# Optimization experiments

Hardware: AMD Instinct MI355X
Metric: run time of the kernel (lower is better)

Reference implementation:

```python
import jax, jax.numpy as jnp
import numpy as np


def gcn_conv(x, src, dst, W, b, N):
    """PyG GCNConv: add self-loops, symmetric D^-1/2 (A+I) D^-1/2 normalization."""
    loop = jnp.arange(N, dtype=src.dtype)
    s = jnp.concatenate([src, loop])
    d = jnp.concatenate([dst, loop])
    deg = jnp.zeros((N,), dtype=x.dtype).at[d].add(1.0)  # in-degree incl. self-loop
    dinv = jax.lax.rsqrt(deg)  # deg >= 1 because of self-loops
    norm = dinv[s] * dinv[d]  # [E+N]
    h = x @ W  # [N, out] linear transform first (as in PyG)
    msg = h[s] * norm[:, None]  # gather + scale
    out = jax.ops.segment_sum(msg, d, num_segments=N)  # scatter-add
    return out + b


def setup_inputs() -> dict:
    key = jax.random.key(0)
    ks = jax.random.split(key, 10)
    N, E, in_dim, h1, h2, A = 100000, 3200000, 256, 32, 64, 64
    x = jax.random.normal(ks[0], (N, in_dim), dtype=jnp.float32)
    ei = jax.random.randint(ks[1], (2, E), 0, N, dtype=jnp.int64)
    def glorot(k, shape):
        lim = float(np.sqrt(6.0 / (shape[0] + shape[1])))
        return jax.random.uniform(k, shape, jnp.float32, -lim, lim)
    return {
        "x": x,
        "ei": ei,
        "num_nodes": N,
        "W1": glorot(ks[2], (in_dim, h1)), "b1": jnp.zeros((h1,), jnp.float32),
        "W2": glorot(ks[3], (h1, h2)),     "b2": jnp.zeros((h2,), jnp.float32),
        "Wo1": glorot(ks[4], (h2, h2)),    "bo1": jnp.zeros((h2,), jnp.float32),
        "Wo2": glorot(ks[5], (h2, A)),     "bo2": jnp.zeros((A,), jnp.float32),
    }


def reference(x, ei, num_nodes, W1, b1, W2, b2, Wo1, bo1, Wo2, bo2):
    src, dst = ei[0], ei[1]
    z = jax.nn.relu(gcn_conv(x, src, dst, W1, b1, num_nodes))
    z = jax.nn.relu(gcn_conv(z, src, dst, W2, b2, num_nodes))
    logits = jax.nn.relu(z @ Wo1 + bo1) @ Wo2 + bo2  # [N, action_space]
    nbatches = z.shape[0] // num_nodes
    # original reshapes with z.size(1)=hidden2 (== action_space here)
    dist = logits.reshape(nbatches, num_nodes * z.shape[1])
    return jax.nn.softmax(dist, axis=-1)  # Categorical probs
```

## Files before the change

### kernel.cpp

```cpp
#include <hip/hip_runtime.h>

#define DEVI __device__ __forceinline__

DEVI unsigned fkey(float f) {
  unsigned u = __float_as_uint(f);
  return u ^ ((u >> 31) ? 0xFFFFFFFFu : 0x80000000u);
}
DEVI float funkey(unsigned k) {
  unsigned b = (k & 0x80000000u) ? (k ^ 0x80000000u) : ~k;
  return __uint_as_float(b);
}
DEVI float f4get(const float4& v, int j) {
  return j == 0 ? v.x : j == 1 ? v.y : j == 2 ? v.z : v.w;
}

constexpr int BSH = 9;
constexpr int BNODES = 1 << BSH;
constexpr int PEPT = 16;
constexpr int PCHUNK = 256 * PEPT;

__global__ void k_binit(int* __restrict__ bcnt) {
  bcnt[threadIdx.x] = 0;
}

__global__ void k_bcount(const int* __restrict__ dst, int* __restrict__ bcnt,
                         int E, int NB) {
  __shared__ int lh[256];
  lh[threadIdx.x] = 0;
  __syncthreads();
  int stride = gridDim.x * 256;
  for (long i = (long)blockIdx.x * 256 + threadIdx.x; i < E; i += stride)
    atomicAdd(&lh[dst[i] >> BSH], 1);
  __syncthreads();
  if (threadIdx.x < NB && lh[threadIdx.x]) atomicAdd(&bcnt[threadIdx.x], lh[threadIdx.x]);
}

__global__ void k_bscan(const int* __restrict__ bcnt, int* __restrict__ bbase,
                        int* __restrict__ bcur, unsigned* __restrict__ scal, int NB) {
  __shared__ int s[256];
  int t = threadIdx.x;
  int v = (t < NB) ? bcnt[t] : 0;
  s[t] = v;
  __syncthreads();
  for (int o = 1; o < 256; o <<= 1) {
    int add = (t >= o) ? s[t - o] : 0;
    __syncthreads();
    s[t] += add;
    __syncthreads();
  }
  int excl = s[t] - v;
  if (t < NB) { bbase[t] = excl; bcur[t] = excl; }
  if (t == 0) { scal[0] = 0u; scal[1] = 0u; }
}

__global__ __launch_bounds__(256)
void k_bpart(const int* __restrict__ src, const int* __restrict__ dst,
             int* __restrict__ bcur, unsigned* __restrict__ epart, int E, int NB) {
  __shared__ int lh[256];
  __shared__ int gbase[256];
  long base = (long)blockIdx.x * PCHUNK;
  lh[threadIdx.x] = 0;
  __syncthreads();
  int ed[PEPT]; int es[PEPT]; unsigned short lpos[PEPT];
#pragma unroll
  for (int j = 0; j < PEPT; j++) {
    long i = base + threadIdx.x + (long)j * 256;
    if (i < E) {
      int d = dst[i];
      es[j] = src[i];
      ed[j] = d;
      lpos[j] = (unsigned short)atomicAdd(&lh[d >> BSH], 1);
    } else {
      ed[j] = -1;
    }
  }
  __syncthreads();
  if (threadIdx.x < NB) {
    int c = lh[threadIdx.x];
    gbase[threadIdx.x] = c ? atomicAdd(&bcur[threadIdx.x], c) : 0;
  }
  __syncthreads();
#pragma unroll
  for (int j = 0; j < PEPT; j++) {
    int d = ed[j];
    if (d >= 0) {
      unsigned p = (unsigned)(gbase[d >> BSH] + (int)lpos[j]);
      epart[p] = ((unsigned)(d & (BNODES - 1)) << 17) | (unsigned)es[j];
    }
  }
}

__global__ __launch_bounds__(256)
void k_fine(const unsigned* __restrict__ epart, const int* __restrict__ bbase,
            const int* __restrict__ bcnt, int* __restrict__ rowptr,
            int* __restrict__ deg, float* __restrict__ dinv,
            int* __restrict__ col, int N) {
  __shared__ int lh[BNODES];
  __shared__ int lexcl[BNODES];
  __shared__ int ssc[256];
  int b = blockIdx.x;
  int base = bbase[b], cnt = bcnt[b];
  int nlo = b << BSH;
  int t = threadIdx.x;
  lh[t] = 0; lh[t + 256] = 0;
  __syncthreads();
  for (int i = t; i < cnt; i += 256) {
    unsigned e = epart[base + i];
    atomicAdd(&lh[e >> 17], 1);
  }
  __syncthreads();
  int a0 = lh[2 * t], a1 = lh[2 * t + 1];
  ssc[t] = a0 + a1;
  __syncthreads();
  for (int o = 1; o < 256; o <<= 1) {
    int add = (t >= o) ? ssc[t - o] : 0;
    __syncthreads();
    ssc[t] += add;
    __syncthreads();
  }
  int excl = ssc[t] - (a0 + a1);
  lexcl[2 * t] = excl;
  lexcl[2 * t + 1] = excl + a0;
  __syncthreads();
#pragma unroll
  for (int k = 0; k < 2; k++) {
    int i = t + k * 256;
    int v = nlo + i;
    if (v < N) {
      int dgv = lh[i];
      deg[v] = dgv;
      rowptr[v] = base + lexcl[i];
      dinv[v] = rsqrtf((float)(dgv + 1));
    }
  }
  __syncthreads();
  lh[2 * t] = lexcl[2 * t];
  lh[2 * t + 1] = lexcl[2 * t + 1];
  __syncthreads();
  for (int i = t; i < cnt; i += 256) {
    unsigned e = epart[base + i];
    int p = atomicAdd(&lh[e >> 17], 1);
    col[base + p] = (int)(e & 0x1FFFFu);
  }
}

__global__ __launch_bounds__(256)
void k_gemm1(const float* __restrict__ in, const float* __restrict__ W,
             const float* __restrict__ dinv, float* __restrict__ out, int N) {
  __shared__ float Wl[256 * 32];
  __shared__ float xb[2][128 * 16];
  const int t = threadIdx.x;

  {
    const float4* W4 = (const float4*)W;
    float4* Wl4 = (float4*)Wl;
#pragma unroll
    for (int i = 0; i < 8; i++) Wl4[t + i * 256] = W4[t + i * 256];
  }

  const int srow = t >> 1;
  const int part = t & 1;
  const int sk = (srow >> 1) & 3;
  long grow = (long)blockIdx.x * 128 + srow;
  const float* gsrc = in + (grow < (long)N ? grow : (long)(N - 1)) * 256 + part * 8;
  const int q0 = part * 2, q1 = part * 2 + 1;
  const int ws0 = srow * 16 + ((q0 ^ sk) << 2);
  const int ws1 = srow * 16 + ((q1 ^ sk) << 2);

  const int cg = t & 3;
  const int rg = t >> 2;
  const int c0 = cg * 8;
  const int rk = (rg >> 1) & 3;

  {
    float4 a = *(const float4*)(gsrc + 0);
    float4 b = *(const float4*)(gsrc + 4);
    *(float4*)&xb[0][ws0] = a;
    *(float4*)&xb[0][ws1] = b;
  }
  __syncthreads();

  float acc[2][8];
#pragma unroll
  for (int i = 0; i < 2; i++)
#pragma unroll
    for (int c = 0; c < 8; c++) acc[i][c] = 0.f;

  for (int ch = 0; ch < 16; ch++) {
    float4 na, nb;
    if (ch < 15) {
      na = *(const float4*)(gsrc + (ch + 1) * 16 + 0);
      nb = *(const float4*)(gsrc + (ch + 1) * 16 + 4);
    }
    const float* xc = xb[ch & 1];
#pragma unroll
    for (int q = 0; q < 4; q++) {
      float4 xv0 = *(const float4*)&xc[rg * 16 + ((q ^ rk) << 2)];
      float4 xv1 = *(const float4*)&xc[(rg + 64) * 16 + ((q ^ rk) << 2)];
#pragma unroll
      for (int jj = 0; jj < 4; jj++) {
        const float* wr = &Wl[(ch * 16 + q * 4 + jj) * 32 + c0];
        float4 wa = *(const float4*)(wr);
        float4 wb = *(const float4*)(wr + 4);
        float x0 = f4get(xv0, jj);
        float x1 = f4get(xv1, jj);
        acc[0][0] = fmaf(x0, wa.x, acc[0][0]);
        acc[0][1] = fmaf(x0, wa.y, acc[0][1]);
        acc[0][2] = fmaf(x0, wa.z, acc[0][2]);
        acc[0][3] = fmaf(x0, wa.w, acc[0][3]);
        acc[0][4] = fmaf(x0, wb.x, acc[0][4]);
        acc[0][5] = fmaf(x0, wb.y, acc[0][5]);
        acc[0][6] = fmaf(x0, wb.z, acc[0][6]);
        acc[0][7] = fmaf(x0, wb.w, acc[0][7]);
        acc[1][0] = fmaf(x1, wa.x, acc[1][0]);
        acc[1][1] = fmaf(x1, wa.y, acc[1][1]);
        acc[1][2] = fmaf(x1, wa.z, acc[1][2]);
        acc[1][3] = fmaf(x1, wa.w, acc[1][3]);
        acc[1][4] = fmaf(x1, wb.x, acc[1][4]);
        acc[1][5] = fmaf(x1, wb.y, acc[1][5]);
        acc[1][6] = fmaf(x1, wb.z, acc[1][6]);
        acc[1][7] = fmaf(x1, wb.w, acc[1][7]);
      }
    }
    if (ch < 15) {
      __syncthreads();
      float* xn = xb[(ch + 1) & 1];
      *(float4*)&xn[ws0] = na;
      *(float4*)&xn[ws1] = nb;
      __syncthreads();
    }
  }

#pragma unroll
  for (int i = 0; i < 2; i++) {
    long r = (long)blockIdx.x * 128 + rg + i * 64;
    if (r < (long)N) {
      float dv = dinv[r];
      float* op = &out[r * 32 + c0];
      *(float4*)(op) = make_float4(acc[i][0] * dv, acc[i][1] * dv,
                                   acc[i][2] * dv, acc[i][3] * dv);
      *(float4*)(op + 4) = make_float4(acc[i][4] * dv, acc[i][5] * dv,
                                       acc[i][6] * dv, acc[i][7] * dv);
    }
  }
}

__global__ __launch_bounds__(256)
void k_head(const float* __restrict__ s2,
            const float* __restrict__ W2, const float* __restrict__ b2,
            const float* __restrict__ Wo1, const float* __restrict__ bo1,
            const float* __restrict__ Wo2, const float* __restrict__ bo2,
            float* __restrict__ out, int N, unsigned* __restrict__ gmax) {
  __shared__ float A[64 * 64];
  __shared__ float B[64 * 64];
  __shared__ float xr[128 * 64];
  const int t = threadIdx.x;
  const int cg = t & 7, rg = t >> 3;
  const int c0 = cg * 8;
  const int key = rg & 7;
  const long r0 = (long)blockIdx.x * 128 + rg * 4;

  {
    const float4* w2 = (const float4*)W2;
    const float4* w1 = (const float4*)Wo1;
    float4* Af = (float4*)A;
    float4* Bf = (float4*)B;
    Af[t] = w2[t];
    Af[t + 256] = w2[t + 256];
#pragma unroll
    for (int i = 0; i < 4; i++) Bf[t + i * 256] = w1[t + i * 256];
  }
  __syncthreads();

  bool rv[4];
  int xrow[4];
#pragma unroll
  for (int i = 0; i < 4; i++) {
    rv[i] = (r0 + i) < (long)N;
    xrow[i] = (rg + 32 * i) * 64;
  }
  const int q0 = (2 * cg) ^ key, q1 = (2 * cg + 1) ^ key;

  float a1[4][8], a2[4][8];

#pragma unroll
  for (int i = 0; i < 4; i++)
#pragma unroll
    for (int c = 0; c < 8; c++) a1[i][c] = 0.f;
  {
    const float* ip = s2 + r0 * 32;
#pragma unroll 2
    for (int k = 0; k < 32; k += 4) {
      float4 xv[4];
#pragma unroll
      for (int i = 0; i < 4; i++)
        xv[i] = rv[i] ? *(const float4*)(ip + i * 32 + k)
                      : make_float4(0.f, 0.f, 0.f, 0.f);
#pragma unroll
      for (int jj = 0; jj < 4; jj++) {
        float4 wa = *(const float4*)&A[(k + jj) * 64 + c0];
        float4 wb = *(const float4*)&A[(k + jj) * 64 + c0 + 4];
#pragma unroll
        for (int i = 0; i < 4; i++) {
          float xs = f4get(xv[i], jj);
          a1[i][0] = fmaf(xs, wa.x, a1[i][0]);
          a1[i][1] = fmaf(xs, wa.y, a1[i][1]);
          a1[i][2] = fmaf(xs, wa.z, a1[i][2]);
          a1[i][3] = fmaf(xs, wa.w, a1[i][3]);
          a1[i][4] = fmaf(xs, wb.x, a1[i][4]);
          a1[i][5] = fmaf(xs, wb.y, a1[i][5]);
          a1[i][6] = fmaf(xs, wb.z, a1[i][6]);
          a1[i][7] = fmaf(xs, wb.w, a1[i][7]);
        }
      }
    }
    float bo[8];
#pragma unroll
    for (int c = 0; c < 8; c++) bo[c] = b2[c0 + c];
#pragma unroll
    for (int i = 0; i < 4; i++) {
      float v0 = fmaxf(a1[i][0] + bo[0], 0.f);
      float v1 = fmaxf(a1[i][1] + bo[1], 0.f);
      float v2 = fmaxf(a1[i][2] + bo[2], 0.f);
      float v3 = fmaxf(a1[i][3] + bo[3], 0.f);
      float v4 = fmaxf(a1[i][4] + bo[4], 0.f);
      float v5 = fmaxf(a1[i][5] + bo[5], 0.f);
      float v6 = fmaxf(a1[i][6] + bo[6], 0.f);
      float v7 = fmaxf(a1[i][7] + bo[7], 0.f);
      *(float4*)&xr[xrow[i] + 4 * q0] = make_float4(v0, v1, v2, v3);
      *(float4*)&xr[xrow[i] + 4 * q1] = make_float4(v4, v5, v6, v7);
    }
  }
  __syncthreads();

  float4 wn[4];
  {
    const float4* w = (const float4*)Wo2;
#pragma unroll
    for (int i = 0; i < 4; i++) wn[i] = w[t + i * 256];
  }

#pragma unroll
  for (int i = 0; i < 4; i++)
#pragma unroll
    for (int c = 0; c < 8; c++) a2[i][c] = 0.f;
#pragma unroll 2
  for (int k = 0; k < 64; k += 4) {
    const int q = k >> 2;
    float4 xv[4];
#pragma unroll
    for (int i = 0; i < 4; i++)
      xv[i] = *(const float4*)&xr[xrow[i] + 4 * (q ^ key)];
#pragma unroll
    for (int jj = 0; jj < 4; jj++) {
      float4 wa = *(const float4*)&B[(k + jj) * 64 + c0];
      float4 wb = *(const float4*)&B[(k + jj) * 64 + c0 + 4];
#pragma unroll
      for (int i = 0; i < 4; i++) {
        float xs = f4get(xv[i], jj);
        a2[i][0] = fmaf(xs, wa.x, a2[i][0]);
        a2[i][1] = fmaf(xs, wa.y, a2[i][1]);
        a2[i][2] = fmaf(xs, wa.z, a2[i][2]);
        a2[i][3] = fmaf(xs, wa.w, a2[i][3]);
        a2[i][4] = fmaf(xs, wb.x, a2[i][4]);
        a2[i][5] = fmaf(xs, wb.y, a2[i][5]);
        a2[i][6] = fmaf(xs, wb.z, a2[i][6]);
        a2[i][7] = fmaf(xs, wb.w, a2[i][7]);
      }
    }
  }
  __syncthreads();

  {
    float4* Af = (float4*)A;
#pragma unroll
    for (int i = 0; i < 4; i++) Af[t + i * 256] = wn[i];
    float bo[8];
#pragma unroll
    for (int c = 0; c < 8; c++) bo[c] = bo1[c0 + c];
#pragma unroll
    for (int i = 0; i < 4; i++) {
      float v0 = fmaxf(a2[i][0] + bo[0], 0.f);
      float v1 = fmaxf(a2[i][1] + bo[1], 0.f);
      float v2 = fmaxf(a2[i][2] + bo[2], 0.f);
      float v3 = fmaxf(a2[i][3] + bo[3], 0.f);
      float v4 = fmaxf(a2[i][4] + bo[4], 0.f);
      float v5 = fmaxf(a2[i][5] + bo[5], 0.f);
      float v6 = fmaxf(a2[i][6] + bo[6], 0.f);
      float v7 = fmaxf(a2[i][7] + bo[7], 0.f);
      *(float4*)&xr[xrow[i] + 4 * q0] = make_float4(v0, v1, v2, v3);
      *(float4*)&xr[xrow[i] + 4 * q1] = make_float4(v4, v5, v6, v7);
    }
  }
  __syncthreads();

#pragma unroll
  for (int i = 0; i < 4; i++)
#pragma unroll
    for (int c = 0; c < 8; c++) a1[i][c] = 0.f;
#pragma unroll 2
  for (int k = 0; k < 64; k += 4) {
    const int q = k >> 2;
    float4 xv[4];
#pragma unroll
    for (int i = 0; i < 4; i++)
      xv[i] = *(const float4*)&xr[xrow[i] + 4 * (q ^ key)];
#pragma unroll
    for (int jj = 0; jj < 4; jj++) {
      float4 wa = *(const float4*)&A[(k + jj) * 64 + c0];
      float4 wb = *(const float4*)&A[(k + jj) * 64 + c0 + 4];
#pragma unroll
      for (int i = 0; i < 4; i++) {
        float xs = f4get(xv[i], jj);
        a1[i][0] = fmaf(xs, wa.x, a1[i][0]);
        a1[i][1] = fmaf(xs, wa.y, a1[i][1]);
        a1[i][2] = fmaf(xs, wa.z, a1[i][2]);
        a1[i][3] = fmaf(xs, wa.w, a1[i][3]);
        a1[i][4] = fmaf(xs, wb.x, a1[i][4]);
        a1[i][5] = fmaf(xs, wb.y, a1[i][5]);
        a1[i][6] = fmaf(xs, wb.z, a1[i][6]);
        a1[i][7] = fmaf(xs, wb.w, a1[i][7]);
      }
    }
  }

  float m = -3.4e38f;
  {
    float bo[8];
#pragma unroll
    for (int c = 0; c < 8; c++) bo[c] = bo2[c0 + c];
#pragma unroll
    for (int i = 0; i < 4; i++) {
      if (!rv[i]) continue;
      float o[8];
#pragma unroll
      for (int c = 0; c < 8; c++) {
        float v = a1[i][c] + bo[c];
        m = fmaxf(m, v);
        o[c] = v;
      }
      float* op = &out[(r0 + i) * 64 + c0];
      *(float4*)(op) = make_float4(o[0], o[1], o[2], o[3]);
      *(float4*)(op + 4) = make_float4(o[4], o[5], o[6], o[7]);
    }
  }
#pragma unroll
  for (int o2 = 1; o2 < 64; o2 <<= 1) m = fmaxf(m, __shfl_xor(m, o2, 64));
  if ((t & 63) == 0) atomicMax(gmax, fkey(m));
}

template <int FEAT, bool BIAS, bool RELU, bool PSCALE>
__launch_bounds__(256)
__global__ void k_aggv(const float* __restrict__ g, const int* __restrict__ col,
                       const int* __restrict__ rowptr, const int* __restrict__ deg,
                       const float* __restrict__ dinv, const float* __restrict__ bias,
                       float* __restrict__ out, int N) {
  constexpr int LPN = FEAT / 4;
  constexpr int NPB = 256 / LPN;
  int nib = threadIdx.x / LPN;
  int c = threadIdx.x % LPN;
  long v = (long)blockIdx.x * NPB + nib;
  if (v >= N) return;

  const float4* g4 = (const float4*)g;
  float4 acc = g4[v * LPN + c];
  int start = rowptr[v], dg = deg[v];
  int e = 0;
  while (e < dg) {
    int cnt = min(LPN, dg - e);
    int idx = (c < cnt) ? col[start + e + c] : 0;
    int j = 0;
    for (; j + 4 <= cnt; j += 4) {
      int u0 = __shfl(idx, j + 0, LPN);
      int u1 = __shfl(idx, j + 1, LPN);
      int u2 = __shfl(idx, j + 2, LPN);
      int u3 = __shfl(idx, j + 3, LPN);
      float4 a0 = g4[(long)u0 * LPN + c];
      float4 a1 = g4[(long)u1 * LPN + c];
      float4 a2 = g4[(long)u2 * LPN + c];
      float4 a3 = g4[(long)u3 * LPN + c];
      acc.x += (a0.x + a1.x) + (a2.x + a3.x);
      acc.y += (a0.y + a1.y) + (a2.y + a3.y);
      acc.z += (a0.z + a1.z) + (a2.z + a3.z);
      acc.w += (a0.w + a1.w) + (a2.w + a3.w);
    }
    for (; j < cnt; j++) {
      int u = __shfl(idx, j, LPN);
      float4 a = g4[(long)u * LPN + c];
      acc.x += a.x; acc.y += a.y; acc.z += a.z; acc.w += a.w;
    }
    e += cnt;
  }
  float dv = dinv[v];
  float4 val;
  val.x = acc.x * dv; val.y = acc.y * dv; val.z = acc.z * dv; val.w = acc.w * dv;
  if (BIAS) {
    float4 b = ((const float4*)bias)[c];
    val.x += b.x; val.y += b.y; val.z += b.z; val.w += b.w;
  }
  if (RELU) {
    val.x = fmaxf(val.x, 0.f); val.y = fmaxf(val.y, 0.f);
    val.z = fmaxf(val.z, 0.f); val.w = fmaxf(val.w, 0.f);
  }
  if (PSCALE) {
    val.x *= dv; val.y *= dv; val.z *= dv; val.w *= dv;
  }
  ((float4*)out)[v * LPN + c] = val;
}

__global__ void k_smsum(const float* __restrict__ logit, unsigned* __restrict__ scal, int total) {
  __shared__ float s[256];
  float gmax = funkey(scal[0]);
  float loc = 0.f;
  for (int i = blockIdx.x * 256 + threadIdx.x; i < total; i += gridDim.x * 256)
    loc += expf(logit[i] - gmax);
  s[threadIdx.x] = loc; __syncthreads();
  for (int o = 128; o > 0; o >>= 1) {
    if (threadIdx.x < o) s[threadIdx.x] += s[threadIdx.x + o];
    __syncthreads();
  }
  if (threadIdx.x == 0) atomicAdd((float*)&scal[1], s[0]);
}

__global__ void k_smnorm(float* __restrict__ logit, const unsigned* __restrict__ scal, int total) {
  float gmax = funkey(scal[0]);
  float inv = 1.0f / __uint_as_float(scal[1]);
  int i = blockIdx.x * 256 + threadIdx.x;
  if (i < total) logit[i] = expf(logit[i] - gmax) * inv;
}

extern "C" void kernel_launch(void* const* d_in, const int* in_sizes, int n_in,
                              void* d_out, int out_size, void* d_ws, size_t ws_size,
                              hipStream_t stream) {
  const float* x   = (const float*)d_in[0];
  const int*   ei  = (const int*)d_in[1];
  const float* W1  = (const float*)d_in[3];
  const float* b1  = (const float*)d_in[4];
  const float* W2  = (const float*)d_in[5];
  const float* b2  = (const float*)d_in[6];
  const float* Wo1 = (const float*)d_in[7];
  const float* bo1 = (const float*)d_in[8];
  const float* Wo2 = (const float*)d_in[9];
  const float* bo2 = (const float*)d_in[10];

  const int N = in_sizes[0] / 256;
  const int E = in_sizes[1] / 2;
  const int* src = ei;
  const int* dst = ei + E;
  const int NB = (N + BNODES - 1) / BNODES;

  size_t o = 0;
  auto carve = [&](size_t bytes) -> char* {
    char* p = (char*)d_ws + o;
    o += (bytes + 255) & ~(size_t)255;
    return p;
  };
  float* R1     = (float*)carve((size_t)N * 64 * 4);
  float* R2     = (float*)carve((size_t)N * 64 * 4);
  int*   col    = (int*)carve((size_t)E * 4);
  int*   deg    = (int*)carve((size_t)N * 4);
  float* dinv   = (float*)carve((size_t)N * 4);
  int*   rowptr = (int*)carve((size_t)N * 4);
  int*   bcnt   = (int*)carve(256 * 4);
  int*   bbase  = (int*)carve(256 * 4);
  int*   bcur   = (int*)carve(256 * 4);
  unsigned* scal = (unsigned*)carve(64);

  unsigned* epart = (unsigned*)R2;
  float* g1 = R1;
  float* p  = R2;
  float* s2 = R1;
  float* logits = (float*)d_out;

  k_binit<<<1, 256, 0, stream>>>(bcnt);
  k_bcount<<<512, 256, 0, stream>>>(dst, bcnt, E, NB);
  k_bscan<<<1, 256, 0, stream>>>(bcnt, bbase, bcur, scal, NB);
  k_bpart<<<(E + PCHUNK - 1) / PCHUNK, 256, 0, stream>>>(src, dst, bcur, epart, E, NB);
  k_fine<<<NB, 256, 0, stream>>>(epart, bbase, bcnt, rowptr, deg, dinv, col, N);

  const int g1G = (N + 127) / 128;
  const int gA  = (N + 31) / 32;

  k_gemm1<<<g1G, 256, 0, stream>>>(x, W1, dinv, g1, N);
  k_aggv<32, true, true, true><<<gA, 256, 0, stream>>>(g1, col, rowptr, deg, dinv, b1, p, N);

  k_aggv<32, false, false, false><<<gA, 256, 0, stream>>>(p, col, rowptr, deg, dinv, nullptr, s2, N);

  k_head<<<g1G, 256, 0, stream>>>(s2, W2, b2, Wo1, bo1, Wo2, bo2, logits, N, scal);

  k_smsum<<<1024, 256, 0, stream>>>(logits, scal, out_size);
  k_smnorm<<<(out_size + 255) / 256, 256, 0, stream>>>(logits, scal, out_size);
}
```

Before: 503.7 us.

## Fuse softmax max/sum into head kernel via per-block online stats

The head kernel now computes a per-block max and sum of exponentials and writes them to a small stats buffer. This replaces the global atomicMax and the separate pass that re-read all the logits to sum the exponentials. A single-block kernel combines the per-block stats with rescaling, and the normalisation pass is vectorised to float4. This removes one full read of the 6.4M-element logit array and the atomics, at the cost of extra exp work and two more syncs inside the head kernel.

Result: faster. 479.5 us (-4.8%).

```diff
diff --git a/kernel.cpp b/kernel.cpp
--- a/kernel.cpp
+++ b/kernel.cpp
@@ -250,7 +250,7 @@
             const float* __restrict__ W2, const float* __restrict__ b2,
             const float* __restrict__ Wo1, const float* __restrict__ bo1,
             const float* __restrict__ Wo2, const float* __restrict__ bo2,
-            float* __restrict__ out, int N, unsigned* __restrict__ gmax) {
+            float* __restrict__ out, int N, float* __restrict__ bstat) {
   __shared__ float A[64 * 64];
   __shared__ float B[64 * 64];
   __shared__ float xr[128 * 64];
@@ -424,29 +424,68 @@
     }
   }
 
+  float bo[8];
+#pragma unroll
+  for (int c = 0; c < 8; c++) bo[c] = bo2[c0 + c];
   float m = -3.4e38f;
-  {
-    float bo[8];
-#pragma unroll
-    for (int c = 0; c < 8; c++) bo[c] = bo2[c0 + c];
-#pragma unroll
-    for (int i = 0; i < 4; i++) {
-      if (!rv[i]) continue;
-      float o[8];
-#pragma unroll
-      for (int c = 0; c < 8; c++) {
-        float v = a1[i][c] + bo[c];
-        m = fmaxf(m, v);
-        o[c] = v;
-      }
-      float* op = &out[(r0 + i) * 64 + c0];
-      *(float4*)(op) = make_float4(o[0], o[1], o[2], o[3]);
-      *(float4*)(op + 4) = make_float4(o[4], o[5], o[6], o[7]);
-    }
+#pragma unroll
+  for (int i = 0; i < 4; i++) {
+    if (!rv[i]) continue;
+    float o[8];
+#pragma unroll
+    for (int c = 0; c < 8; c++) {
+      float v = a1[i][c] + bo[c];
+      m = fmaxf(m, v);
+      o[c] = v;
+    }
+    float* op = &out[(r0 + i) * 64 + c0];
+    *(float4*)(op) = make_float4(o[0], o[1], o[2], o[3]);
+    *(float4*)(op + 4) = make_float4(o[4], o[5], o[6], o[7]);
   }
 #pragma unroll
   for (int o2 = 1; o2 < 64; o2 <<= 1) m = fmaxf(m, __shfl_xor(m, o2, 64));
-  if ((t & 63) == 0) atomicMax(gmax, fkey(m));
+  __syncthreads();
+  if ((t & 63) == 0) xr[t >> 6] = m;
+  __syncthreads();
+  const float lm = fmaxf(fmaxf(xr[0], xr[1]), fmaxf(xr[2], xr[3]));
+  float ls = 0.f;
+#pragma unroll
+  for (int i = 0; i < 4; i++) {
+    if (!rv[i]) continue;
+#pragma unroll
+    for (int c = 0; c < 8; c++) ls += expf(a1[i][c] + bo[c] - lm);
+  }
+#pragma unroll
+  for (int o2 = 1; o2 < 64; o2 <<= 1) ls += __shfl_xor(ls, o2, 64);
+  if ((t & 63) == 0) xr[8 + (t >> 6)] = ls;
+  __syncthreads();
+  if (t == 0) {
+    bstat[2 * blockIdx.x] = lm;
+    bstat[2 * blockIdx.x + 1] = xr[8] + xr[9] + xr[10] + xr[11];
+  }
+}
+
+__global__ void k_smfin(const float* __restrict__ bstat, int nb,
+                        unsigned* __restrict__ scal) {
+  __shared__ float s[64];
+  int t = threadIdx.x;
+  float lm = -3.4e38f;
+  for (int i = t; i < nb; i += 256) lm = fmaxf(lm, bstat[2 * i]);
+#pragma unroll
+  for (int o = 1; o < 64; o <<= 1) lm = fmaxf(lm, __shfl_xor(lm, o, 64));
+  if ((t & 63) == 0) s[t >> 6] = lm;
+  __syncthreads();
+  float gm = fmaxf(fmaxf(s[0], s[1]), fmaxf(s[2], s[3]));
+  float ls = 0.f;
+  for (int i = t; i < nb; i += 256) ls += bstat[2 * i + 1] * expf(bstat[2 * i] - gm);
+#pragma unroll
+  for (int o = 1; o < 64; o <<= 1) ls += __shfl_xor(ls, o, 64);
+  if ((t & 63) == 0) s[4 + (t >> 6)] = ls;
+  __syncthreads();
+  if (t == 0) {
+    scal[0] = __float_as_uint(gm);
+    scal[1] = __float_as_uint(s[4] + s[5] + s[6] + s[7]);
+  }
 }
 
 template <int FEAT, bool BIAS, bool RELU, bool PSCALE>
@@ -508,25 +547,19 @@
   ((float4*)out)[v * LPN + c] = val;
 }
 
-__global__ void k_smsum(const float* __restrict__ logit, unsigned* __restrict__ scal, int total) {
-  __shared__ float s[256];
-  float gmax = funkey(scal[0]);
-  float loc = 0.f;
-  for (int i = blockIdx.x * 256 + threadIdx.x; i < total; i += gridDim.x * 256)
-    loc += expf(logit[i] - gmax);
-  s[threadIdx.x] = loc; __syncthreads();
-  for (int o = 128; o > 0; o >>= 1) {
-    if (threadIdx.x < o) s[threadIdx.x] += s[threadIdx.x + o];
-    __syncthreads();
-  }
-  if (threadIdx.x == 0) atomicAdd((float*)&scal[1], s[0]);
-}
-
-__global__ void k_smnorm(float* __restrict__ logit, const unsigned* __restrict__ scal, int total) {
-  float gmax = funkey(scal[0]);
+__global__ void k_smnorm(float4* __restrict__ logit, const unsigned* __restrict__ scal,
+                         int total4) {
+  float gmax = __uint_as_float(scal[0]);
   float inv = 1.0f / __uint_as_float(scal[1]);
   int i = blockIdx.x * 256 + threadIdx.x;
-  if (i < total) logit[i] = expf(logit[i] - gmax) * inv;
+  if (i < total4) {
+    float4 v = logit[i];
+    v.x = expf(v.x - gmax) * inv;
+    v.y = expf(v.y - gmax) * inv;
+    v.z = expf(v.z - gmax) * inv;
+    v.w = expf(v.w - gmax) * inv;
+    logit[i] = v;
+  }
 }
 
 extern "C" void kernel_launch(void* const* d_in, const int* in_sizes, int n_in,
@@ -565,6 +598,7 @@
   int*   bbase  = (int*)carve(256 * 4);
   int*   bcur   = (int*)carve(256 * 4);
   unsigned* scal = (unsigned*)carve(64);
+  float* bstat  = (float*)carve(8192);
 
   unsigned* epart = (unsigned*)R2;
   float* g1 = R1;
@@ -586,8 +620,8 @@
 
   k_aggv<32, false, false, false><<<gA, 256, 0, stream>>>(p, col, rowptr, deg, dinv, nullptr, s2, N);
 
-  k_head<<<g1G, 256, 0, stream>>>(s2, W2, b2, Wo1, bo1, Wo2, bo2, logits, N, scal);
-
-  k_smsum<<<1024, 256, 0, stream>>>(logits, scal, out_size);
-  k_smnorm<<<(out_size + 255) / 256, 256, 0, stream>>>(logits, scal, out_size);
-}
+  k_head<<<g1G, 256, 0, stream>>>(s2, W2, b2, Wo1, bo1, Wo2, bo2, logits, N, bstat);
+
+  k_smfin<<<1, 256, 0, stream>>>(bstat, g1G, scal);
+  k_smnorm<<<(out_size / 4 + 255) / 256, 256, 0, stream>>>((float4*)logits, scal, out_size / 4);
+}
```
